# Optimization experiments

Hardware: AMD Instinct MI355X
Metric: run time of the kernel (lower is better)

Reference implementation:

```python
import jax, jax.numpy as jnp
import numpy as np

B, P, CD, V = 4096, 64, 2, 3
D, K, H, L, S, NI, NF = 128, 2048, 256, 5, 4, 100000, 10
COMMIT = 0.25
IN_DIM = CD + CD * 2 * NF  # 42


def _lin(k, out, inn):
    kw, kb = jax.random.split(k)
    lim = 1.0 / np.sqrt(inn)
    W = jax.random.uniform(kw, (out, inn), jnp.float32, -lim, lim)
    b = jax.random.uniform(kb, (out,), jnp.float32, -lim, lim)
    return W, b


def setup_inputs() -> dict:
    key = jax.random.key(0)
    ks = jax.random.split(key, 8)
    coords = jax.random.uniform(ks[0], (B, P, CD), jnp.float32) * 2.0 - 1.0
    latent_indices = jax.random.randint(ks[1], (B,), 0, NI)
    latents = jax.random.normal(ks[2], (NI, S, D), jnp.float32)
    emb = jax.random.normal(ks[3], (S, K, D), jnp.float32)
    vq_emb = emb / jnp.linalg.norm(emb, axis=-1, keepdims=True)
    mod = [_lin(jax.random.fold_in(ks[4], i), H, D) for i in range(L)]
    mod_W = jnp.stack([w for w, _ in mod])
    mod_b = jnp.stack([b for _, b in mod])
    dec_W0, dec_b0 = _lin(ks[5], H, IN_DIM)
    hid = [_lin(jax.random.fold_in(ks[6], i), H, H) for i in range(L - 1)]
    dec_Wh = jnp.stack([w for w, _ in hid])
    dec_bh = jnp.stack([b for _, b in hid])
    last_W, last_b = _lin(ks[7], V, H)
    return dict(coords=coords, latent_indices=latent_indices, latents=latents,
                vq_emb=vq_emb, mod_W=mod_W, mod_b=mod_b,
                dec_W0=dec_W0, dec_b0=dec_b0, dec_Wh=dec_Wh, dec_bh=dec_bh,
                last_W=last_W, last_b=last_b)


def reference(coords, latent_indices, latents, vq_emb, mod_W, mod_b,
              dec_W0, dec_b0, dec_Wh, dec_bh, last_W, last_b):
    sg = jax.lax.stop_gradient
    img_lat = latents[latent_indices]  # (B, S, D) gather from large table
    z_q_sum = jnp.zeros((B, D), coords.dtype)
    residual = jnp.zeros((B, D), coords.dtype)
    total_vq_loss = jnp.zeros((), coords.dtype)
    for s in range(S):  # sequential residual VQ stages (structural, S=4)
        z_stage = img_lat[:, s, :]
        if s == 0:
            residual = z_stage
            z_cur = z_stage
        else:
            residual = residual + z_stage
            z_cur = residual - sg(z_q_sum)
        emb = vq_emb[s]  # (K, D)
        # squared distances via expansion: ||z||^2 - 2 z e^T + ||e||^2
        dists = (jnp.sum(z_cur * z_cur, axis=1, keepdims=True)
                 - 2.0 * z_cur @ emb.T
                 + jnp.sum(emb * emb, axis=1))  # (B, K)
        idx = jnp.argmin(dists, axis=1)  # (B,)
        z_q = emb[idx]  # (B, D) codebook gather
        z_q_st = z_cur + sg(z_q - z_cur)  # straight-through
        total_vq_loss = total_vq_loss + COMMIT * jnp.mean((sg(z_q) - z_cur) ** 2)
        z_q_sum = z_q_sum + z_q_st
    # FiLM betas: (L, B, H)
    betas = jnp.einsum('lhd,bd->lbh', mod_W, z_q_sum) + mod_b[:, None, :]
    # positional encoding: concat[x, sin(x*2^f*pi), cos(x*2^f*pi)]
    freqs = (2.0 ** jnp.arange(NF, dtype=coords.dtype)) * np.pi  # (NF,)
    xe = coords[..., None] * freqs  # (B, P, CD, NF)
    enc = jnp.concatenate([coords,
                           jnp.sin(xe).reshape(B, P, -1),
                           jnp.cos(xe).reshape(B, P, -1)], axis=-1)  # (B,P,42)
    x = jax.nn.relu(jnp.einsum('bpi,hi->bph', enc, dec_W0) + dec_b0
                    + betas[0][:, None, :])
    for i in range(1, L):
        x = jax.nn.relu(jnp.einsum('bph,gh->bpg', x, dec_Wh[i - 1]) + dec_bh[i - 1]
                        + betas[i][:, None, :])
    values = jnp.einsum('bph,vh->bpv', x, last_W) + last_b  # (B, P, V)
    return values, total_vq_loss
```

## Files before the change

### kernel.cpp

```cpp
#include <hip/hip_runtime.h>

typedef unsigned short u16;
typedef unsigned int u32;
typedef __attribute__((ext_vector_type(8))) short short8;
typedef __attribute__((ext_vector_type(4))) float f32x4;

__device__ __forceinline__ float b2f(u16 u) {
    return __builtin_bit_cast(float, (u32)u << 16);
}
__device__ __forceinline__ u16 f2b(float f) {
    u32 x = __builtin_bit_cast(u32, f);
    x += 0x7fffu + ((x >> 16) & 1u);
    return (u16)(x >> 16);
}

#define WS_LPART  0
#define WS_ENORM  512
#define WS_ZQSUM  8704
#define WS_BETAS  532992
#define WS_W0PAD  3154432
#define WS_DWH    3162624
#define WS_VQH    WS_BETAS
#define WS_VQL    (WS_BETAS + 524288)

__global__ __launch_bounds__(64) void enorm_kernel(const float* __restrict__ vq,
                                                   float* __restrict__ enorm) {
    int code = blockIdx.x;
    int lane = threadIdx.x;
    const float* e = vq + (size_t)code * 128;
    float a = e[lane], b = e[lane + 64];
    float v = a * a + b * b;
    #pragma unroll
    for (int off = 32; off; off >>= 1) v += __shfl_down(v, off);
    if (lane == 0) enorm[code] = v;
}

__global__ __launch_bounds__(256) void vqsplit_kernel(const float* __restrict__ vq,
                                                      u16* __restrict__ vh,
                                                      u16* __restrict__ vl) {
    int i = blockIdx.x * 256 + threadIdx.x;
    float v = vq[i];
    u16 h = f2b(v);
    vh[i] = h;
    vl[i] = f2b(v - b2f(h));
}

__global__ __launch_bounds__(256) void padw0_kernel(const float* __restrict__ W0,
                                                    u16* __restrict__ w0pad) {
    int i = blockIdx.x * 256 + threadIdx.x;
    int row = i >> 6, k = i & 63;
    w0pad[i] = (k < 42) ? f2b(W0[row * 42 + k]) : (u16)0;
}

__global__ __launch_bounds__(256) void dwh_kernel(const float* __restrict__ Wh,
                                                  u16* __restrict__ dwh) {
    int i = blockIdx.x * 256 + threadIdx.x;
    dwh[i] = f2b(Wh[i]);
}

__global__ __launch_bounds__(512, 2) void vq_kernel(const int* __restrict__ lidx,
                                                    const float* __restrict__ latents,
                                                    const float* __restrict__ vq,
                                                    const u16* __restrict__ vqh,
                                                    const u16* __restrict__ vql,
                                                    const float* __restrict__ enorm,
                                                    float* __restrict__ zqsum_g,
                                                    float* __restrict__ lpartial) {
    int tid = threadIdx.x;
    int wv = tid >> 6;
    int lane = tid & 63;
    int col = lane & 15;
    int g = lane >> 4;
    int urow = tid >> 5;
    int uc = tid & 31;

    __shared__ __align__(16) float s_resid[16][132];
    __shared__ __align__(16) float s_zqsum[16][132];
    __shared__ __align__(16) float s_zcur[16][132];
    __shared__ float rd1[32][16], rd2[32][16];
    __shared__ int   ri1[32][16], ri2[32][16];
    __shared__ int   sel[16];
    __shared__ float lossb[8];

    size_t li_u = (size_t)lidx[blockIdx.x * 16 + urow];

    {
        float4 v = ((const float4*)latents)[li_u * 128 + uc];
        *(float4*)&s_resid[urow][uc * 4] = v;
        *(float4*)&s_zcur[urow][uc * 4]  = v;
        float4 z = {0.f, 0.f, 0.f, 0.f};
        *(float4*)&s_zqsum[urow][uc * 4] = z;
    }
    float loss_local = 0.f;
    __syncthreads();

    for (int s = 0; s < 4; ++s) {
        short8 bh[4], bl[4];
        #pragma unroll
        for (int kc4 = 0; kc4 < 4; ++kc4) {
            int kk = kc4 * 32 + g * 8;
            float4 z0 = *(const float4*)&s_zcur[col][kk];
            float4 z1 = *(const float4*)&s_zcur[col][kk + 4];
            float zz[8] = {z0.x, z0.y, z0.z, z0.w, z1.x, z1.y, z1.z, z1.w};
            short8 h8, l8;
            #pragma unroll
            for (int j = 0; j < 8; ++j) {
                u16 hb = f2b(zz[j]);
                h8[j] = (short)hb;
                l8[j] = (short)f2b(zz[j] - b2f(hb));
            }
            bh[kc4] = h8; bl[kc4] = l8;
        }

        const u16* baseh = vqh + ((size_t)(s * 2048 + wv * 256 + col)) * 128 + g * 8;
        const u16* basel = vql + ((size_t)(s * 2048 + wv * 256 + col)) * 128 + g * 8;
        const float* enb = enorm + s * 2048 + wv * 256 + g * 4;

        float b1 = 3.4e38f, b2v = 3.4e38f; int i1 = 0, i2 = 0;
        auto top2 = [&](float dv, int kv) {
            if (dv < b1)       { b2v = b1; i2 = i1; b1 = dv; i1 = kv; }
            else if (dv < b2v) { b2v = dv; i2 = kv; }
        };

        for (int tp = 0; tp < 8; ++tp) {
            const u16* phA = baseh + (size_t)tp * 32 * 128;
            const u16* plA = basel + (size_t)tp * 32 * 128;
            short8 ahA[4], alA[4], ahB[4], alB[4];
            #pragma unroll
            for (int kc4 = 0; kc4 < 4; ++kc4) {
                ahA[kc4] = *(const short8*)&phA[kc4 * 32];
                alA[kc4] = *(const short8*)&plA[kc4 * 32];
                ahB[kc4] = *(const short8*)&phA[16 * 128 + kc4 * 32];
                alB[kc4] = *(const short8*)&plA[16 * 128 + kc4 * 32];
            }
            f32x4 accA = {0.f, 0.f, 0.f, 0.f};
            f32x4 accB = {0.f, 0.f, 0.f, 0.f};
            #pragma unroll
            for (int kc4 = 0; kc4 < 4; ++kc4) {
                accA = __builtin_amdgcn_mfma_f32_16x16x32_bf16(ahA[kc4], bh[kc4], accA, 0, 0, 0);
                accB = __builtin_amdgcn_mfma_f32_16x16x32_bf16(ahB[kc4], bh[kc4], accB, 0, 0, 0);
                accA = __builtin_amdgcn_mfma_f32_16x16x32_bf16(ahA[kc4], bl[kc4], accA, 0, 0, 0);
                accB = __builtin_amdgcn_mfma_f32_16x16x32_bf16(ahB[kc4], bl[kc4], accB, 0, 0, 0);
                accA = __builtin_amdgcn_mfma_f32_16x16x32_bf16(alA[kc4], bh[kc4], accA, 0, 0, 0);
                accB = __builtin_amdgcn_mfma_f32_16x16x32_bf16(alB[kc4], bh[kc4], accB, 0, 0, 0);
            }
            float4 enA = *(const float4*)&enb[tp * 32];
            float4 enB = *(const float4*)&enb[tp * 32 + 16];
            int kA = wv * 256 + tp * 32 + g * 4;
            int kB = kA + 16;
            top2(enA.x - 2.f * accA[0], kA + 0);
            top2(enA.y - 2.f * accA[1], kA + 1);
            top2(enA.z - 2.f * accA[2], kA + 2);
            top2(enA.w - 2.f * accA[3], kA + 3);
            top2(enB.x - 2.f * accB[0], kB + 0);
            top2(enB.y - 2.f * accB[1], kB + 1);
            top2(enB.z - 2.f * accB[2], kB + 2);
            top2(enB.w - 2.f * accB[3], kB + 3);
        }
        int slot = wv * 4 + g;
        rd1[slot][col] = b1; rd2[slot][col] = b2v;
        ri1[slot][col] = i1; ri2[slot][col] = i2;
        __syncthreads();

        if (tid < 16) {
            float m1 = 3.4e38f, m2 = 3.4e38f; int j1 = 0, j2 = 0;
            for (int sl = 0; sl < 32; ++sl) {
                float d1c = rd1[sl][tid], d2c = rd2[sl][tid];
                int   k1 = ri1[sl][tid], k2 = ri2[sl][tid];
                if (d1c < m1) {
                    float n2; int n2i;
                    if (m1 <= d2c) { n2 = m1; n2i = j1; } else { n2 = d2c; n2i = k2; }
                    m1 = d1c; j1 = k1; m2 = n2; j2 = n2i;
                } else if (d1c < m2) { m2 = d1c; j2 = k1; }
            }
            int jw = j1;
            if (m2 - m1 < 1e-2f) {
                const float* e1p = vq + ((size_t)s * 2048 + j1) * 128;
                const float* e2p = vq + ((size_t)s * 2048 + j2) * 128;
                double t1 = 0.0, t2 = 0.0;
                for (int d = 0; d < 128; ++d) {
                    double z  = (double)s_zcur[tid][d];
                    double e1 = (double)e1p[d], e2 = (double)e2p[d];
                    t1 += e1 * e1 - 2.0 * e1 * z;
                    t2 += e2 * e2 - 2.0 * e2 * z;
                }
                if (t2 < t1 || (t2 == t1 && j2 < j1)) jw = j2;
            }
            sel[tid] = jw;
        }
        __syncthreads();

        {
            int k = sel[urow];
            float4 e = ((const float4*)vq)[((size_t)s * 2048 + k) * 32 + uc];
            int d = uc * 4;
            float4 z4 = *(const float4*)&s_zcur[urow][d];
            float f0 = e.x - z4.x, f1 = e.y - z4.y;
            float f2v = e.z - z4.z, f3 = e.w - z4.w;
            loss_local += f0 * f0 + f1 * f1 + f2v * f2v + f3 * f3;
            float4 zq = *(float4*)&s_zqsum[urow][d];
            zq.x += e.x; zq.y += e.y; zq.z += e.z; zq.w += e.w;
            *(float4*)&s_zqsum[urow][d] = zq;
            if (s < 3) {
                float4 lv = ((const float4*)latents)[li_u * 128 + (size_t)(s + 1) * 32 + uc];
                float4 rs = *(float4*)&s_resid[urow][d];
                rs.x += lv.x; rs.y += lv.y; rs.z += lv.z; rs.w += lv.w;
                *(float4*)&s_resid[urow][d] = rs;
                float4 zcn;
                zcn.x = rs.x - zq.x; zcn.y = rs.y - zq.y;
                zcn.z = rs.z - zq.z; zcn.w = rs.w - zq.w;
                *(float4*)&s_zcur[urow][d] = zcn;
            }
        }
        __syncthreads();
    }

    ((float4*)zqsum_g)[((size_t)blockIdx.x * 16 + urow) * 32 + uc] =
        *(const float4*)&s_zqsum[urow][uc * 4];

    #pragma unroll
    for (int off = 32; off; off >>= 1) loss_local += __shfl_down(loss_local, off);
    if (lane == 0) lossb[wv] = loss_local;
    __syncthreads();
    if (tid == 0) {
        float l = 0.f;
        #pragma unroll
        for (int i = 0; i < 8; ++i) l += lossb[i];
        lpartial[blockIdx.x] = l;
    }
}

__global__ __launch_bounds__(128) void betas_kernel(const float* __restrict__ zqsum,
                                                    const float* __restrict__ mod_W,
                                                    const float* __restrict__ mod_b,
                                                    u16* __restrict__ betas) {
    int bg = blockIdx.x, l = blockIdx.y, t = threadIdx.x;
    __shared__ float zq[16][128];
    for (int u = t; u < 2048; u += 128) ((float*)zq)[u] = zqsum[(size_t)bg * 2048 + u];
    __syncthreads();

    float acc0[16], acc1[16];
    #pragma unroll
    for (int i = 0; i < 16; ++i) { acc0[i] = 0.f; acc1[i] = 0.f; }

    const float4* w0 = (const float4*)(mod_W + ((size_t)l * 256 + t) * 128);
    const float4* w1 = (const float4*)(mod_W + ((size_t)l * 256 + t + 128) * 128);
    #pragma unroll
    for (int c = 0; c < 32; ++c) {
        float4 wa = w0[c], wb = w1[c];
        #pragma unroll
        for (int bb = 0; bb < 16; ++bb) {
            float4 za = *(const float4*)&zq[bb][c * 4];
            acc0[bb] += wa.x * za.x + wa.y * za.y + wa.z * za.z + wa.w * za.w;
            acc1[bb] += wb.x * za.x + wb.y * za.y + wb.z * za.z + wb.w * za.w;
        }
    }
    float bias0 = mod_b[l * 256 + t], bias1 = mod_b[l * 256 + t + 128];
    #pragma unroll
    for (int bb = 0; bb < 16; ++bb) {
        size_t o = ((size_t)l * 4096 + bg * 16 + bb) * 256;
        betas[o + t]       = f2b(acc0[bb] + bias0);
        betas[o + t + 128] = f2b(acc1[bb] + bias1);
    }
}

template<int KD>
__device__ __forceinline__ void gemm_run(const u16* __restrict__ wl, const int wstride,
                                         const u16* __restrict__ xb, const int colsw,
                                         f32x4 acc[4][4]) {
    constexpr int NIT = KD / 32;
    short8 a[2][4], bf[2][4];
    #pragma unroll
    for (int nt = 0; nt < 4; ++nt)
        a[0][nt] = *(const short8*)&wl[(size_t)nt * 16 * wstride];
    #pragma unroll
    for (int mt = 0; mt < 4; ++mt)
        bf[0][mt] = *(const short8*)&xb[mt * 16 * 256 + colsw];
    #pragma unroll
    for (int it = 0; it < NIT; ++it) {
        constexpr int B0 = 0;
        const int cur = it & 1, nxt = cur ^ 1;
        (void)B0;
        if (it + 1 < NIT) {
            const int kc = (it + 1) * 32;
            #pragma unroll
            for (int nt = 0; nt < 4; ++nt)
                a[nxt][nt] = *(const short8*)&wl[(size_t)nt * 16 * wstride + kc];
            #pragma unroll
            for (int mt = 0; mt < 4; ++mt)
                bf[nxt][mt] = *(const short8*)&xb[mt * 16 * 256 + (kc ^ colsw)];
        }
        #pragma unroll
        for (int nt = 0; nt < 4; ++nt)
            #pragma unroll
            for (int mt = 0; mt < 4; ++mt)
                acc[nt][mt] = __builtin_amdgcn_mfma_f32_16x16x32_bf16(
                    a[cur][nt], bf[cur][mt], acc[nt][mt], 0, 0, 0);
    }
}

__global__ __launch_bounds__(256, 3) void mlp_kernel(const float* __restrict__ coords,
                                                     const u16* __restrict__ w0pad,
                                                     const float* __restrict__ dec_b0,
                                                     const u16* __restrict__ dwh,
                                                     const float* __restrict__ dec_bh,
                                                     const float* __restrict__ last_W,
                                                     const float* __restrict__ last_b,
                                                     const u16* __restrict__ betas,
                                                     float* __restrict__ out) {
    __shared__ __align__(16) u16 X[64 * 256];
    int b = blockIdx.x;
    int tid = threadIdx.x;
    int lane = tid & 63, wv = tid >> 6;
    int q = lane >> 4, r16 = lane & 15;
    int nbase = wv * 64;
    int swr = (r16 & 7) << 3;
    int colsw = (q * 8) ^ swr;

    auto xput = [&](int m, int c, u16 val) {
        X[m * 256 + (c ^ ((m & 7) << 3))] = val;
    };

    {
        int m = tid & 63, g = tid >> 6;
        float c0 = coords[((b << 6) + m) * 2 + 0];
        float c1 = coords[((b << 6) + m) * 2 + 1];
        if (g == 0) {
            xput(m, 0, f2b(c0)); xput(m, 1, f2b(c1));
            #pragma unroll
            for (int c = 42; c < 64; ++c) xput(m, c, 0);
            #pragma unroll
            for (int f = 0; f < 10; ++f) {
                float pf = 3.14159265358979323846f * (float)(1 << f);
                xput(m, 32 + f, f2b(cosf(c1 * pf)));
            }
        } else if (g == 1) {
            #pragma unroll
            for (int f = 0; f < 10; ++f) {
                float pf = 3.14159265358979323846f * (float)(1 << f);
                xput(m, 2 + f, f2b(sinf(c0 * pf)));
            }
        } else if (g == 2) {
            #pragma unroll
            for (int f = 0; f < 10; ++f) {
                float pf = 3.14159265358979323846f * (float)(1 << f);
                xput(m, 12 + f, f2b(sinf(c1 * pf)));
            }
        } else {
            #pragma unroll
            for (int f = 0; f < 10; ++f) {
                float pf = 3.14159265358979323846f * (float)(1 << f);
                xput(m, 22 + f, f2b(cosf(c0 * pf)));
            }
        }
    }
    __syncthreads();

    f32x4 acc[4][4];
    const u16* xb = X + r16 * 256;

    auto zero_acc = [&]() {
        #pragma unroll
        for (int nt = 0; nt < 4; ++nt)
            #pragma unroll
            for (int mt = 0; mt < 4; ++mt) {
                f32x4 z = {0.f, 0.f, 0.f, 0.f};
                acc[nt][mt] = z;
            }
    };

    auto epilogue = [&](const float* bias, const u16* beta_l) {
        float bv[4][4];
        #pragma unroll
        for (int nt = 0; nt < 4; ++nt) {
            int n0 = nbase + nt * 16 + q * 4;
            float4 bs = *(const float4*)&bias[n0];
            ushort4 bt = *(const ushort4*)&beta_l[n0];
            bv[nt][0] = bs.x + b2f(bt.x);
            bv[nt][1] = bs.y + b2f(bt.y);
            bv[nt][2] = bs.z + b2f(bt.z);
            bv[nt][3] = bs.w + b2f(bt.w);
        }
        __syncthreads();
        #pragma unroll
        for (int mt = 0; mt < 4; ++mt) {
            int m = mt * 16 + r16;
            #pragma unroll
            for (int nt = 0; nt < 4; ++nt) {
                int n0 = nbase + nt * 16 + q * 4;
                float v0 = fmaxf(acc[nt][mt][0] + bv[nt][0], 0.f);
                float v1 = fmaxf(acc[nt][mt][1] + bv[nt][1], 0.f);
                float v2 = fmaxf(acc[nt][mt][2] + bv[nt][2], 0.f);
                float v3 = fmaxf(acc[nt][mt][3] + bv[nt][3], 0.f);
                uint2 pk;
                pk.x = (u32)f2b(v0) | ((u32)f2b(v1) << 16);
                pk.y = (u32)f2b(v2) | ((u32)f2b(v3) << 16);
                *(uint2*)&X[m * 256 + (n0 ^ swr)] = pk;
            }
        }
        __syncthreads();
    };

    zero_acc();
    gemm_run<64>(w0pad + (size_t)(nbase + r16) * 64 + q * 8, 64, xb, colsw, acc);
    epilogue(dec_b0, betas + (size_t)b * 256);

    #pragma unroll
    for (int l = 1; l < 5; ++l) {
        zero_acc();
        gemm_run<256>(dwh + (size_t)(l - 1) * 65536 + (size_t)(nbase + r16) * 256 + q * 8,
                      256, xb, colsw, acc);
        epilogue(dec_bh + (size_t)(l - 1) * 256, betas + ((size_t)l * 4096 + b) * 256);
    }

    {
        const u16* xt = X + (wv * 16 + r16) * 256;
        const float* lwp = last_W + r16 * 256 + q * 8;
        f32x4 tacc = {0.f, 0.f, 0.f, 0.f};
        #pragma unroll
        for (int kc = 0; kc < 256; kc += 32) {
            short8 xf = *(const short8*)&xt[kc ^ colsw];
            short8 wh, wl8;
            if (r16 < 3) {
                float4 wa = *(const float4*)&lwp[kc];
                float4 wb = *(const float4*)&lwp[kc + 4];
                float ww[8] = {wa.x, wa.y, wa.z, wa.w, wb.x, wb.y, wb.z, wb.w};
                #pragma unroll
                for (int j = 0; j < 8; ++j) {
                    u16 hb = f2b(ww[j]);
                    wh[j]  = (short)hb;
                    wl8[j] = (short)f2b(ww[j] - b2f(hb));
                }
            } else {
                #pragma unroll
                for (int j = 0; j < 8; ++j) { wh[j] = 0; wl8[j] = 0; }
            }
            tacc = __builtin_amdgcn_mfma_f32_16x16x32_bf16(wh,  xf, tacc, 0, 0, 0);
            tacc = __builtin_amdgcn_mfma_f32_16x16x32_bf16(wl8, xf, tacc, 0, 0, 0);
        }
        __syncthreads();
        float* fbuf = (float*)X;
        if (lane < 16) {
            int rr = wv * 16 + lane;
            fbuf[rr * 3 + 0] = tacc[0] + last_b[0];
            fbuf[rr * 3 + 1] = tacc[1] + last_b[1];
            fbuf[rr * 3 + 2] = tacc[2] + last_b[2];
        }
        __syncthreads();
        if (tid < 192) out[(size_t)b * 192 + tid] = fbuf[tid];
    }
}

__global__ __launch_bounds__(64) void finalize_kernel(const float* __restrict__ lpartial,
                                                      float* __restrict__ out) {
    int t = threadIdx.x;
    float s = 0.f;
    for (int i = t; i < 256; i += 64) s += lpartial[i];
    #pragma unroll
    for (int off = 32; off; off >>= 1) s += __shfl_down(s, off);
    if (t == 0) out[786432] = 0.25f * s * (1.f / (4096.f * 128.f));
}

extern "C" void kernel_launch(void* const* d_in, const int* in_sizes, int n_in,
                              void* d_out, int out_size, void* d_ws, size_t ws_size,
                              hipStream_t stream) {
    const float* coords  = (const float*)d_in[0];
    const int*   lidx    = (const int*)d_in[1];
    const float* latents = (const float*)d_in[2];
    const float* vq      = (const float*)d_in[3];
    const float* mod_W   = (const float*)d_in[4];
    const float* mod_b   = (const float*)d_in[5];
    const float* dec_W0  = (const float*)d_in[6];
    const float* dec_b0  = (const float*)d_in[7];
    const float* dec_Wh  = (const float*)d_in[8];
    const float* dec_bh  = (const float*)d_in[9];
    const float* last_W  = (const float*)d_in[10];
    const float* last_b  = (const float*)d_in[11];
    float* out = (float*)d_out;

    float* wsf      = (float*)d_ws;
    float* lpartial = wsf + WS_LPART;
    float* enorm    = wsf + WS_ENORM;
    float* zqsum    = wsf + WS_ZQSUM;
    u16*   betas    = (u16*)(wsf + WS_BETAS);
    u16*   w0pad    = (u16*)(wsf + WS_W0PAD);
    u16*   dwh      = (u16*)(wsf + WS_DWH);
    u16*   vqh      = (u16*)(wsf + WS_VQH);
    u16*   vql      = (u16*)(wsf + WS_VQL);

    enorm_kernel<<<8192, 64, 0, stream>>>(vq, enorm);
    vqsplit_kernel<<<4096, 256, 0, stream>>>(vq, vqh, vql);
    padw0_kernel<<<64, 256, 0, stream>>>(dec_W0, w0pad);
    dwh_kernel<<<1024, 256, 0, stream>>>(dec_Wh, dwh);
    vq_kernel<<<256, 512, 0, stream>>>(lidx, latents, vq, vqh, vql, enorm, zqsum, lpartial);
    betas_kernel<<<dim3(256, 5), 128, 0, stream>>>(zqsum, mod_W, mod_b, betas);
    mlp_kernel<<<4096, 256, 0, stream>>>(coords, w0pad, dec_b0, dwh, dec_bh,
                                         last_W, last_b, betas, out);
    finalize_kernel<<<1, 64, 0, stream>>>(lpartial, out);
}
```

Measured before the change: 797.0 us.

## Fuse prep kernels and double per-block wave count in VQ and MLP kernels

Merges the four weight/codebook preprocessing kernels into one launch to cut launch overhead. The VQ kernel goes to 1024 threads so each wave scans 128 codes instead of 256, and the MLP kernel goes to 512 threads with each wave owning 32 output columns. The MLP GEMM drops its register double-buffering and uses a packed bf16 convert instruction in the epilogue. More waves per block should raise occupancy and latency hiding, at the cost of less work per wave, a longer top-2 reduction, and losing the explicit prefetch.

Result: no change. 786.5 us (-1.3%).

```diff
diff --git a/kernel.cpp b/kernel.cpp
--- a/kernel.cpp
+++ b/kernel.cpp
@@ -23,49 +23,49 @@
 #define WS_VQH    WS_BETAS
 #define WS_VQL    (WS_BETAS + 524288)
 
-__global__ __launch_bounds__(64) void enorm_kernel(const float* __restrict__ vq,
-                                                   float* __restrict__ enorm) {
-    int code = blockIdx.x;
-    int lane = threadIdx.x;
-    const float* e = vq + (size_t)code * 128;
-    float a = e[lane], b = e[lane + 64];
-    float v = a * a + b * b;
-    #pragma unroll
-    for (int off = 32; off; off >>= 1) v += __shfl_down(v, off);
-    if (lane == 0) enorm[code] = v;
-}
-
-__global__ __launch_bounds__(256) void vqsplit_kernel(const float* __restrict__ vq,
-                                                      u16* __restrict__ vh,
-                                                      u16* __restrict__ vl) {
-    int i = blockIdx.x * 256 + threadIdx.x;
-    float v = vq[i];
-    u16 h = f2b(v);
-    vh[i] = h;
-    vl[i] = f2b(v - b2f(h));
-}
-
-__global__ __launch_bounds__(256) void padw0_kernel(const float* __restrict__ W0,
-                                                    u16* __restrict__ w0pad) {
-    int i = blockIdx.x * 256 + threadIdx.x;
-    int row = i >> 6, k = i & 63;
-    w0pad[i] = (k < 42) ? f2b(W0[row * 42 + k]) : (u16)0;
-}
-
-__global__ __launch_bounds__(256) void dwh_kernel(const float* __restrict__ Wh,
-                                                  u16* __restrict__ dwh) {
-    int i = blockIdx.x * 256 + threadIdx.x;
-    dwh[i] = f2b(Wh[i]);
-}
-
-__global__ __launch_bounds__(512, 2) void vq_kernel(const int* __restrict__ lidx,
-                                                    const float* __restrict__ latents,
-                                                    const float* __restrict__ vq,
-                                                    const u16* __restrict__ vqh,
-                                                    const u16* __restrict__ vql,
-                                                    const float* __restrict__ enorm,
-                                                    float* __restrict__ zqsum_g,
-                                                    float* __restrict__ lpartial) {
+__global__ __launch_bounds__(256) void prep_kernel(const float* __restrict__ vq,
+                                                   const float* __restrict__ W0,
+                                                   const float* __restrict__ Wh,
+                                                   float* __restrict__ enorm,
+                                                   u16* __restrict__ vh,
+                                                   u16* __restrict__ vl,
+                                                   u16* __restrict__ w0pad,
+                                                   u16* __restrict__ dwh) {
+    int bx = blockIdx.x;
+    int tid = threadIdx.x;
+    if (bx < 2048) {
+        int code = bx * 4 + (tid >> 6);
+        int lane = tid & 63;
+        const float* e = vq + (size_t)code * 128;
+        float a = e[lane], b = e[lane + 64];
+        float v = a * a + b * b;
+        #pragma unroll
+        for (int off = 32; off; off >>= 1) v += __shfl_down(v, off);
+        if (lane == 0) enorm[code] = v;
+    } else if (bx < 2048 + 4096) {
+        int i = (bx - 2048) * 256 + tid;
+        float v = vq[i];
+        u16 h = f2b(v);
+        vh[i] = h;
+        vl[i] = f2b(v - b2f(h));
+    } else if (bx < 2048 + 4096 + 64) {
+        int i = (bx - 6144) * 256 + tid;
+        int row = i >> 6, k = i & 63;
+        w0pad[i] = (k < 42) ? f2b(W0[row * 42 + k]) : (u16)0;
+    } else {
+        int i = (bx - 6208) * 256 + tid;
+        dwh[i] = f2b(Wh[i]);
+    }
+}
+
+__global__ __launch_bounds__(1024, 4) void vq_kernel(const int* __restrict__ lidx,
+                                                     const float* __restrict__ latents,
+                                                     const float* __restrict__ vq,
+                                                     const u16* __restrict__ vqh,
+                                                     const u16* __restrict__ vql,
+                                                     const float* __restrict__ enorm,
+                                                     float* __restrict__ zqsum_g,
+                                                     float* __restrict__ lpartial) {
     int tid = threadIdx.x;
     int wv = tid >> 6;
     int lane = tid & 63;
@@ -77,14 +77,14 @@
     __shared__ __align__(16) float s_resid[16][132];
     __shared__ __align__(16) float s_zqsum[16][132];
     __shared__ __align__(16) float s_zcur[16][132];
-    __shared__ float rd1[32][16], rd2[32][16];
-    __shared__ int   ri1[32][16], ri2[32][16];
+    __shared__ float rd1[64][16], rd2[64][16];
+    __shared__ int   ri1[64][16], ri2[64][16];
     __shared__ int   sel[16];
-    __shared__ float lossb[8];
-
-    size_t li_u = (size_t)lidx[blockIdx.x * 16 + urow];
-
-    {
+    __shared__ float lossb[16];
+
+    size_t li_u = 0;
+    if (tid < 512) {
+        li_u = (size_t)lidx[blockIdx.x * 16 + urow];
         float4 v = ((const float4*)latents)[li_u * 128 + uc];
         *(float4*)&s_resid[urow][uc * 4] = v;
         *(float4*)&s_zcur[urow][uc * 4]  = v;
@@ -112,9 +112,9 @@
             bh[kc4] = h8; bl[kc4] = l8;
         }
 
-        const u16* baseh = vqh + ((size_t)(s * 2048 + wv * 256 + col)) * 128 + g * 8;
-        const u16* basel = vql + ((size_t)(s * 2048 + wv * 256 + col)) * 128 + g * 8;
-        const float* enb = enorm + s * 2048 + wv * 256 + g * 4;
+        const u16* baseh = vqh + ((size_t)(s * 2048 + wv * 128 + col)) * 128 + g * 8;
+        const u16* basel = vql + ((size_t)(s * 2048 + wv * 128 + col)) * 128 + g * 8;
+        const float* enb = enorm + s * 2048 + wv * 128 + g * 4;
 
         float b1 = 3.4e38f, b2v = 3.4e38f; int i1 = 0, i2 = 0;
         auto top2 = [&](float dv, int kv) {
@@ -122,40 +122,29 @@
             else if (dv < b2v) { b2v = dv; i2 = kv; }
         };
 
-        for (int tp = 0; tp < 8; ++tp) {
-            const u16* phA = baseh + (size_t)tp * 32 * 128;
-            const u16* plA = basel + (size_t)tp * 32 * 128;
-            short8 ahA[4], alA[4], ahB[4], alB[4];
+        #pragma unroll 2
+        for (int t = 0; t < 8; ++t) {
+            const u16* ph = baseh + (size_t)t * 16 * 128;
+            const u16* pl = basel + (size_t)t * 16 * 128;
+            short8 ah[4], al[4];
             #pragma unroll
             for (int kc4 = 0; kc4 < 4; ++kc4) {
-                ahA[kc4] = *(const short8*)&phA[kc4 * 32];
-                alA[kc4] = *(const short8*)&plA[kc4 * 32];
-                ahB[kc4] = *(const short8*)&phA[16 * 128 + kc4 * 32];
-                alB[kc4] = *(const short8*)&plA[16 * 128 + kc4 * 32];
-            }
-            f32x4 accA = {0.f, 0.f, 0.f, 0.f};
-            f32x4 accB = {0.f, 0.f, 0.f, 0.f};
+                ah[kc4] = *(const short8*)&ph[kc4 * 32];
+                al[kc4] = *(const short8*)&pl[kc4 * 32];
+            }
+            f32x4 a = {0.f, 0.f, 0.f, 0.f};
             #pragma unroll
             for (int kc4 = 0; kc4 < 4; ++kc4) {
-                accA = __builtin_amdgcn_mfma_f32_16x16x32_bf16(ahA[kc4], bh[kc4], accA, 0, 0, 0);
-                accB = __builtin_amdgcn_mfma_f32_16x16x32_bf16(ahB[kc4], bh[kc4], accB, 0, 0, 0);
-                accA = __builtin_amdgcn_mfma_f32_16x16x32_bf16(ahA[kc4], bl[kc4], accA, 0, 0, 0);
-                accB = __builtin_amdgcn_mfma_f32_16x16x32_bf16(ahB[kc4], bl[kc4], accB, 0, 0, 0);
-                accA = __builtin_amdgcn_mfma_f32_16x16x32_bf16(alA[kc4], bh[kc4], accA, 0, 0, 0);
-                accB = __builtin_amdgcn_mfma_f32_16x16x32_bf16(alB[kc4], bh[kc4], accB, 0, 0, 0);
-            }
-            float4 enA = *(const float4*)&enb[tp * 32];
-            float4 enB = *(const float4*)&enb[tp * 32 + 16];
-            int kA = wv * 256 + tp * 32 + g * 4;
-            int kB = kA + 16;
-            top2(enA.x - 2.f * accA[0], kA + 0);
-            top2(enA.y - 2.f * accA[1], kA + 1);
-            top2(enA.z - 2.f * accA[2], kA + 2);
-            top2(enA.w - 2.f * accA[3], kA + 3);
-            top2(enB.x - 2.f * accB[0], kB + 0);
-            top2(enB.y - 2.f * accB[1], kB + 1);
-            top2(enB.z - 2.f * accB[2], kB + 2);
-            top2(enB.w - 2.f * accB[3], kB + 3);
+                a = __builtin_amdgcn_mfma_f32_16x16x32_bf16(ah[kc4], bh[kc4], a, 0, 0, 0);
+                a = __builtin_amdgcn_mfma_f32_16x16x32_bf16(ah[kc4], bl[kc4], a, 0, 0, 0);
+                a = __builtin_amdgcn_mfma_f32_16x16x32_bf16(al[kc4], bh[kc4], a, 0, 0, 0);
+            }
+            float4 en = *(const float4*)&enb[t * 16];
+            int kT = wv * 128 + t * 16 + g * 4;
+            top2(en.x - 2.f * a[0], kT + 0);
+            top2(en.y - 2.f * a[1], kT + 1);
+            top2(en.z - 2.f * a[2], kT + 2);
+            top2(en.w - 2.f * a[3], kT + 3);
         }
         int slot = wv * 4 + g;
         rd1[slot][col] = b1; rd2[slot][col] = b2v;
@@ -164,7 +153,7 @@
 
         if (tid < 16) {
             float m1 = 3.4e38f, m2 = 3.4e38f; int j1 = 0, j2 = 0;
-            for (int sl = 0; sl < 32; ++sl) {
+            for (int sl = 0; sl < 64; ++sl) {
                 float d1c = rd1[sl][tid], d2c = rd2[sl][tid];
                 int   k1 = ri1[sl][tid], k2 = ri2[sl][tid];
                 if (d1c < m1) {
@@ -190,7 +179,7 @@
         }
         __syncthreads();
 
-        {
+        if (tid < 512) {
             int k = sel[urow];
             float4 e = ((const float4*)vq)[((size_t)s * 2048 + k) * 32 + uc];
             int d = uc * 4;
@@ -215,8 +204,9 @@
         __syncthreads();
     }
 
-    ((float4*)zqsum_g)[((size_t)blockIdx.x * 16 + urow) * 32 + uc] =
-        *(const float4*)&s_zqsum[urow][uc * 4];
+    if (tid < 512)
+        ((float4*)zqsum_g)[((size_t)blockIdx.x * 16 + urow) * 32 + uc] =
+            *(const float4*)&s_zqsum[urow][uc * 4];
 
     #pragma unroll
     for (int off = 32; off; off >>= 1) loss_local += __shfl_down(loss_local, off);
@@ -225,7 +215,7 @@
     if (tid == 0) {
         float l = 0.f;
         #pragma unroll
-        for (int i = 0; i < 8; ++i) l += lossb[i];
+        for (int i = 0; i < 16; ++i) l += lossb[i];
         lpartial[blockIdx.x] = l;
     }
 }
@@ -267,39 +257,27 @@
 template<int KD>
 __device__ __forceinline__ void gemm_run(const u16* __restrict__ wl, const int wstride,
                                          const u16* __restrict__ xb, const int colsw,
-                                         f32x4 acc[4][4]) {
-    constexpr int NIT = KD / 32;
-    short8 a[2][4], bf[2][4];
-    #pragma unroll
-    for (int nt = 0; nt < 4; ++nt)
-        a[0][nt] = *(const short8*)&wl[(size_t)nt * 16 * wstride];
-    #pragma unroll
-    for (int mt = 0; mt < 4; ++mt)
-        bf[0][mt] = *(const short8*)&xb[mt * 16 * 256 + colsw];
-    #pragma unroll
-    for (int it = 0; it < NIT; ++it) {
-        constexpr int B0 = 0;
-        const int cur = it & 1, nxt = cur ^ 1;
-        (void)B0;
-        if (it + 1 < NIT) {
-            const int kc = (it + 1) * 32;
-            #pragma unroll
-            for (int nt = 0; nt < 4; ++nt)
-                a[nxt][nt] = *(const short8*)&wl[(size_t)nt * 16 * wstride + kc];
-            #pragma unroll
-            for (int mt = 0; mt < 4; ++mt)
-                bf[nxt][mt] = *(const short8*)&xb[mt * 16 * 256 + (kc ^ colsw)];
-        }
-        #pragma unroll
-        for (int nt = 0; nt < 4; ++nt)
+                                         f32x4 acc[2][4]) {
+    #pragma unroll
+    for (int it = 0; it < KD / 32; ++it) {
+        const int kc = it * 32;
+        short8 a[2], bf[4];
+        #pragma unroll
+        for (int nt = 0; nt < 2; ++nt)
+            a[nt] = *(const short8*)&wl[(size_t)nt * 16 * wstride + kc];
+        #pragma unroll
+        for (int mt = 0; mt < 4; ++mt)
+            bf[mt] = *(const short8*)&xb[mt * 16 * 256 + (kc ^ colsw)];
+        #pragma unroll
+        for (int nt = 0; nt < 2; ++nt)
             #pragma unroll
             for (int mt = 0; mt < 4; ++mt)
                 acc[nt][mt] = __builtin_amdgcn_mfma_f32_16x16x32_bf16(
-                    a[cur][nt], bf[cur][mt], acc[nt][mt], 0, 0, 0);
-    }
-}
-
-__global__ __launch_bounds__(256, 3) void mlp_kernel(const float* __restrict__ coords,
+                    a[nt], bf[mt], acc[nt][mt], 0, 0, 0);
+    }
+}
+
+__global__ __launch_bounds__(512, 4) void mlp_kernel(const float* __restrict__ coords,
                                                      const u16* __restrict__ w0pad,
                                                      const float* __restrict__ dec_b0,
                                                      const u16* __restrict__ dwh,
@@ -313,55 +291,56 @@
     int tid = threadIdx.x;
     int lane = tid & 63, wv = tid >> 6;
     int q = lane >> 4, r16 = lane & 15;
-    int nbase = wv * 64;
+    int nbase = wv * 32;
     int swr = (r16 & 7) << 3;
     int colsw = (q * 8) ^ swr;
 
-    auto xput = [&](int m, int c, u16 val) {
-        X[m * 256 + (c ^ ((m & 7) << 3))] = val;
-    };
-
     {
         int m = tid & 63, g = tid >> 6;
-        float c0 = coords[((b << 6) + m) * 2 + 0];
-        float c1 = coords[((b << 6) + m) * 2 + 1];
-        if (g == 0) {
-            xput(m, 0, f2b(c0)); xput(m, 1, f2b(c1));
-            #pragma unroll
-            for (int c = 42; c < 64; ++c) xput(m, c, 0);
-            #pragma unroll
-            for (int f = 0; f < 10; ++f) {
-                float pf = 3.14159265358979323846f * (float)(1 << f);
-                xput(m, 32 + f, f2b(cosf(c1 * pf)));
-            }
-        } else if (g == 1) {
-            #pragma unroll
-            for (int f = 0; f < 10; ++f) {
-                float pf = 3.14159265358979323846f * (float)(1 << f);
-                xput(m, 2 + f, f2b(sinf(c0 * pf)));
-            }
-        } else if (g == 2) {
-            #pragma unroll
-            for (int f = 0; f < 10; ++f) {
-                float pf = 3.14159265358979323846f * (float)(1 << f);
-                xput(m, 12 + f, f2b(sinf(c1 * pf)));
-            }
-        } else {
-            #pragma unroll
-            for (int f = 0; f < 10; ++f) {
-                float pf = 3.14159265358979323846f * (float)(1 << f);
-                xput(m, 22 + f, f2b(cosf(c0 * pf)));
+        auto xput = [&](int mm, int c, u16 val) {
+            X[mm * 256 + (c ^ ((mm & 7) << 3))] = val;
+        };
+        if (g < 4) {
+            float c0 = coords[(((size_t)b << 6) + m) * 2 + 0];
+            float c1 = coords[(((size_t)b << 6) + m) * 2 + 1];
+            if (g == 0) {
+                xput(m, 0, f2b(c0)); xput(m, 1, f2b(c1));
+                #pragma unroll
+                for (int c = 42; c < 64; ++c) xput(m, c, 0);
+                #pragma unroll
+                for (int f = 0; f < 10; ++f) {
+                    float pf = 3.14159265358979323846f * (float)(1 << f);
+                    xput(m, 32 + f, f2b(cosf(c1 * pf)));
+                }
+            } else if (g == 1) {
+                #pragma unroll
+                for (int f = 0; f < 10; ++f) {
+                    float pf = 3.14159265358979323846f * (float)(1 << f);
+                    xput(m, 2 + f, f2b(sinf(c0 * pf)));
+                }
+            } else if (g == 2) {
+                #pragma unroll
+                for (int f = 0; f < 10; ++f) {
+                    float pf = 3.14159265358979323846f * (float)(1 << f);
+                    xput(m, 12 + f, f2b(sinf(c1 * pf)));
+                }
+            } else {
+                #pragma unroll
+                for (int f = 0; f < 10; ++f) {
+                    float pf = 3.14159265358979323846f * (float)(1 << f);
+                    xput(m, 22 + f, f2b(cosf(c0 * pf)));
+                }
             }
         }
     }
     __syncthreads();
 
-    f32x4 acc[4][4];
+    f32x4 acc[2][4];
     const u16* xb = X + r16 * 256;
 
     auto zero_acc = [&]() {
         #pragma unroll
-        for (int nt = 0; nt < 4; ++nt)
+        for (int nt = 0; nt < 2; ++nt)
             #pragma unroll
             for (int mt = 0; mt < 4; ++mt) {
                 f32x4 z = {0.f, 0.f, 0.f, 0.f};
@@ -370,9 +349,9 @@
     };
 
     auto epilogue = [&](const float* bias, const u16* beta_l) {
-        float bv[4][4];
-        #pragma unroll
-        for (int nt = 0; nt < 4; ++nt) {
+        float bv[2][4];
+        #pragma unroll
+        for (int nt = 0; nt < 2; ++nt) {
             int n0 = nbase + nt * 16 + q * 4;
             float4 bs = *(const float4*)&bias[n0];
             ushort4 bt = *(const ushort4*)&beta_l[n0];
@@ -386,15 +365,15 @@
         for (int mt = 0; mt < 4; ++mt) {
             int m = mt * 16 + r16;
             #pragma unroll
-            for (int nt = 0; nt < 4; ++nt) {
+            for (int nt = 0; nt < 2; ++nt) {
                 int n0 = nbase + nt * 16 + q * 4;
                 float v0 = fmaxf(acc[nt][mt][0] + bv[nt][0], 0.f);
                 float v1 = fmaxf(acc[nt][mt][1] + bv[nt][1], 0.f);
                 float v2 = fmaxf(acc[nt][mt][2] + bv[nt][2], 0.f);
                 float v3 = fmaxf(acc[nt][mt][3] + bv[nt][3], 0.f);
                 uint2 pk;
-                pk.x = (u32)f2b(v0) | ((u32)f2b(v1) << 16);
-                pk.y = (u32)f2b(v2) | ((u32)f2b(v3) << 16);
+                asm("v_cvt_pk_bf16_f32 %0, %1, %2" : "=v"(pk.x) : "v"(v0), "v"(v1));
+                asm("v_cvt_pk_bf16_f32 %0, %1, %2" : "=v"(pk.y) : "v"(v2), "v"(v3));
                 *(uint2*)&X[m * 256 + (n0 ^ swr)] = pk;
             }
         }
@@ -413,10 +392,10 @@
         epilogue(dec_bh + (size_t)(l - 1) * 256, betas + ((size_t)l * 4096 + b) * 256);
     }
 
-    {
+    f32x4 tacc = {0.f, 0.f, 0.f, 0.f};
+    if (wv < 4) {
         const u16* xt = X + (wv * 16 + r16) * 256;
         const float* lwp = last_W + r16 * 256 + q * 8;
-        f32x4 tacc = {0.f, 0.f, 0.f, 0.f};
         #pragma unroll
         for (int kc = 0; kc < 256; kc += 32) {
             short8 xf = *(const short8*)&xt[kc ^ colsw];
@@ -438,9 +417,11 @@
             tacc = __builtin_amdgcn_mfma_f32_16x16x32_bf16(wh,  xf, tacc, 0, 0, 0);
             tacc = __builtin_amdgcn_mfma_f32_16x16x32_bf16(wl8, xf, tacc, 0, 0, 0);
         }
-        __syncthreads();
+    }
+    __syncthreads();
+    {
         float* fbuf = (float*)X;
-        if (lane < 16) {
+        if (wv < 4 && lane < 16) {
             int rr = wv * 16 + lane;
             fbuf[rr * 3 + 0] = tacc[0] + last_b[0];
             fbuf[rr * 3 + 1] = tacc[1] + last_b[1];
@@ -488,13 +469,10 @@
     u16*   vqh      = (u16*)(wsf + WS_VQH);
     u16*   vql      = (u16*)(wsf + WS_VQL);
 
-    enorm_kernel<<<8192, 64, 0, stream>>>(vq, enorm);
-    vqsplit_kernel<<<4096, 256, 0, stream>>>(vq, vqh, vql);
-    padw0_kernel<<<64, 256, 0, stream>>>(dec_W0, w0pad);
-    dwh_kernel<<<1024, 256, 0, stream>>>(dec_Wh, dwh);
-    vq_kernel<<<256, 512, 0, stream>>>(lidx, latents, vq, vqh, vql, enorm, zqsum, lpartial);
+    prep_kernel<<<7232, 256, 0, stream>>>(vq, dec_W0, dec_Wh, enorm, vqh, vql, w0pad, dwh);
+    vq_kernel<<<256, 1024, 0, stream>>>(lidx, latents, vq, vqh, vql, enorm, zqsum, lpartial);
     betas_kernel<<<dim3(256, 5), 128, 0, stream>>>(zqsum, mod_W, mod_b, betas);
-    mlp_kernel<<<4096, 256, 0, stream>>>(coords, w0pad, dec_b0, dwh, dec_bh,
+    mlp_kernel<<<4096, 512, 0, stream>>>(coords, w0pad, dec_b0, dwh, dec_bh,
                                          last_W, last_b, betas, out);
     finalize_kernel<<<1, 64, 0, stream>>>(lpartial, out);
 }
```
